# Performance work log

Hardware: AMD Instinct MI355X
Metric: run time of the kernel (lower is better)

## Reference

```python
import jax, jax.numpy as jnp
import numpy as np


def setup_inputs() -> dict:
    key = jax.random.key(0)
    k1, k2, k3, k4 = jax.random.split(key, 4)
    B, T, F, U = 64, 1024, 256, 512
    x = jax.random.normal(k1, (B, T, F), dtype=jnp.float32)
    # small init scale keeps the linear-activation cell state numerically tame
    kernel = jax.random.normal(k2, (F, 4 * U), dtype=jnp.float32) * 0.05
    recurrent_kernel = jax.random.normal(k3, (U, 4 * U), dtype=jnp.float32) * 0.05
    bias = jax.random.normal(k4, (4 * U,), dtype=jnp.float32) * 0.05
    return {"x": x, "kernel": kernel, "recurrent_kernel": recurrent_kernel, "bias": bias}


def reference(x, kernel, recurrent_kernel, bias):
    # Keras LSTM with activation=None (linear candidate / linear output),
    # recurrent_activation=sigmoid, gate order [i, f, c, o]; then external tanh.
    B, T, F = x.shape
    U = recurrent_kernel.shape[0]
    # precompute input projections for all timesteps: [T, B, 4U]
    xz = jnp.einsum('btf,fg->tbg', x, kernel) + bias

    def step(carry, xz_t):
        h, c = carry
        z = xz_t + h @ recurrent_kernel  # [B, 4U]
        i, f, g, o = jnp.split(z, 4, axis=-1)
        i = jax.nn.sigmoid(i)
        f = jax.nn.sigmoid(f)
        o = jax.nn.sigmoid(o)
        c = f * c + i * g          # candidate activation is linear (None)
        h = o * c                  # output activation is linear (None)
        return (h, c), h

    h0 = jnp.zeros((B, U), dtype=x.dtype)
    c0 = jnp.zeros((B, U), dtype=x.dtype)
    (_, _), hs = jax.lax.scan(step, (h0, c0), xz)  # hs: [T, B, U]
    seq = jnp.swapaxes(hs, 0, 1)  # [B, T, U] (return_sequences=True)
    return jnp.tanh(seq)          # external activation applied post-hoc
```

## Files before the change

### kernel.cpp

```cpp
#include <hip/hip_runtime.h>
#include <stdint.h>


#define Tt   1024
#define Uu   512
#define G4U  2048
#define NWG  256
#define NTHR 128
#define TAGSTRIDE 16

#define WF_ELEMS (2 * 24 * 64 * 8)
#define WF_BYTES (WF_ELEMS * 2)
#define ZB_PLANE (16 * 17)
#define SMEM_BYTES (WF_BYTES + 4 * ZB_PLANE * 4)

typedef short  bf16x8 __attribute__((ext_vector_type(8)));
typedef float  f32x4  __attribute__((ext_vector_type(4)));
typedef int    int4v  __attribute__((ext_vector_type(4)));
typedef unsigned int u32;

__device__ __forceinline__ unsigned short f2bf(float f) {
  u32 u = __builtin_bit_cast(u32, f);
  u += 0x7fffu + ((u >> 16) & 1u);
  return (unsigned short)(u >> 16);
}

__device__ __forceinline__ int4v load16_ag(const unsigned short* p) {
  int4v r;
  asm volatile("global_load_dwordx4 %0, %1, off sc1"
               : "=v"(r) : "v"(p) : "memory");
  return r;
}
__device__ __forceinline__ void store2_ag(unsigned short* p, unsigned short v) {
  asm volatile("global_store_short %0, %1, off sc1"
               :: "v"(p), "v"((u32)v) : "memory");
}
__device__ __forceinline__ void store4_ag(u32* p, u32 v) {
  asm volatile("global_store_dword %0, %1, off sc1"
               :: "v"(p), "v"(v) : "memory");
}
__device__ __forceinline__ u32 load_tag_wait(const u32* p) {
  u32 r;
  asm volatile("global_load_dword %0, %1, off sc1\n\ts_waitcnt vmcnt(0)"
               : "=v"(r) : "v"(p) : "memory");
  return r;
}

__device__ __forceinline__ float sigf(float z) {
  return __builtin_amdgcn_rcpf(1.f + __expf(-z));
}
__device__ __forceinline__ float tanh_fast(float v) {
  const float e = __expf(-2.f * fabsf(v));
  const float r = (1.f - e) * __builtin_amdgcn_rcpf(1.f + e);
  return copysignf(r, v);
}

extern "C" __global__ void __launch_bounds__(NTHR, 1)
lstm_persistent(const float* __restrict__ x,
                const float* __restrict__ Wk,
                const float* __restrict__ Rk,
                const float* __restrict__ bias,
                float* __restrict__ out,
                unsigned short* __restrict__ hbuf,
                u32* __restrict__ tags)
{
  extern __shared__ char smem[];
  unsigned short* wf   = (unsigned short*)smem;
  float*          zbuf = (float*)(smem + WF_BYTES);

  const int bid = blockIdx.x;
  const int tid = threadIdx.x;
  const int w   = tid >> 6;
  const int l   = tid & 63;
  const int g   = bid & 3;
  const int m   = bid >> 2;

  for (int i = tid; i < WF_ELEMS; i += NTHR) {
    const int j    = i & 7;
    const int lane = (i >> 3) & 63;
    const int kt   = (i >> 9) % 24;
    const int nt   = (i >> 9) / 24;
    const int k    = kt * 32 + ((lane >> 4) << 3) + j;
    const int n    = nt * 16 + (lane & 15);
    const int zc   = (n >> 3) * Uu + m * 8 + (n & 7);
    const float v  = (k < 256) ? Wk[(size_t)k * G4U + zc]
                               : Rk[(size_t)(k - 256) * G4U + zc];
    wf[i] = f2bf(v);
  }
  __syncthreads();

  bf16x8 wfx[4][2];
  #pragma unroll
  for (int q = 0; q < 4; ++q)
    #pragma unroll
    for (int nt = 0; nt < 2; ++nt)
      wfx[q][nt] = *(const bf16x8*)(wf + (((nt * 24) + (2 * q + w)) * 64 + l) * 8);

  const int row_c = tid >> 3;
  const int uu    = tid & 7;
  const int b_out = g * 16 + row_c;
  const int u_out = m * 8 + uu;
  float breg[4];
  #pragma unroll
  for (int gg = 0; gg < 4; ++gg) breg[gg] = bias[gg * Uu + u_out];
  float creg = 0.f;

  const int b_ld = g * 16 + (l & 15);
  const int kq   = (l >> 4) * 8;
  const u32* tagp = tags + ((size_t)g * 64 + l) * TAGSTRIDE;

  for (int t = 0; t < Tt; ++t) {
    u32 tv = (u32)t;
    if (w == 0)
      asm volatile("global_load_dword %0, %1, off sc1"
                   : "=v"(tv) : "v"(tagp) : "memory");

    f32x4 aX0 = {0.f, 0.f, 0.f, 0.f};
    f32x4 aX1 = {0.f, 0.f, 0.f, 0.f};
    const float* xp = x + ((size_t)b_ld * Tt + t) * 256 + kq;
    #pragma unroll
    for (int q = 0; q < 4; ++q) {
      const int kt = 2 * q + w;
      const float4 v0 = *(const float4*)(xp + kt * 32);
      const float4 v1 = *(const float4*)(xp + kt * 32 + 4);
      int r0, r1, r2, r3;
      asm("v_cvt_pk_bf16_f32 %0, %1, %2" : "=v"(r0) : "v"(v0.x), "v"(v0.y));
      asm("v_cvt_pk_bf16_f32 %0, %1, %2" : "=v"(r1) : "v"(v0.z), "v"(v0.w));
      asm("v_cvt_pk_bf16_f32 %0, %1, %2" : "=v"(r2) : "v"(v1.x), "v"(v1.y));
      asm("v_cvt_pk_bf16_f32 %0, %1, %2" : "=v"(r3) : "v"(v1.z), "v"(v1.w));
      const int4v ai = {r0, r1, r2, r3};
      const bf16x8 a = __builtin_bit_cast(bf16x8, ai);
      aX0 = __builtin_amdgcn_mfma_f32_16x16x32_bf16(a, wfx[q][0], aX0, 0, 0, 0);
      aX1 = __builtin_amdgcn_mfma_f32_16x16x32_bf16(a, wfx[q][1], aX1, 0, 0, 0);
    }

    asm volatile("s_waitcnt vmcnt(0)" ::: "memory");
    __builtin_amdgcn_sched_barrier(0);
    if (w == 0) {
      while (!__all(tv >= (u32)t)) {
        __builtin_amdgcn_s_sleep(1);
        tv = load_tag_wait(tagp);
        __builtin_amdgcn_sched_barrier(0);
      }
    }
    __builtin_amdgcn_s_barrier();
    __builtin_amdgcn_sched_barrier(0);

    const unsigned short* hrow =
        hbuf + ((size_t)(t & 1) * 64 + b_ld) * Uu + kq;
    int4v hf[8];
    #pragma unroll
    for (int q = 0; q < 8; ++q)
      hf[q] = load16_ag(hrow + (2 * q + w) * 32);
    asm volatile("s_waitcnt vmcnt(0)" ::: "memory");
    __builtin_amdgcn_sched_barrier(0);

    f32x4 aH0 = {0.f, 0.f, 0.f, 0.f};
    f32x4 aH1 = {0.f, 0.f, 0.f, 0.f};
    #pragma unroll
    for (int q = 0; q < 8; ++q) {
      const int kt = 8 + 2 * q + w;
      const bf16x8 a = __builtin_bit_cast(bf16x8, hf[q]);
      const bf16x8 b0 = *(const bf16x8*)(wf + ((0 * 24 + kt) * 64 + l) * 8);
      const bf16x8 b1 = *(const bf16x8*)(wf + ((1 * 24 + kt) * 64 + l) * 8);
      aH0 = __builtin_amdgcn_mfma_f32_16x16x32_bf16(a, b0, aH0, 0, 0, 0);
      aH1 = __builtin_amdgcn_mfma_f32_16x16x32_bf16(a, b1, aH1, 0, 0, 0);
    }

    const f32x4 z0 = aX0 + aH0;
    const f32x4 z1 = aX1 + aH1;

    __syncthreads();
    {
      float* zb = zbuf + ((w * 2 + 0) * 16 + (l >> 4) * 4) * 17 + (l & 15);
      #pragma unroll
      for (int r = 0; r < 4; ++r) {
        zb[r * 17]           = z0[r];
        zb[r * 17 + 16 * 17] = z1[r];
      }
    }
    __syncthreads();

    float z[4];
    #pragma unroll
    for (int gg = 0; gg < 4; ++gg) {
      const int n  = gg * 8 + uu;
      const int nt = n >> 4, nc = n & 15;
      z[gg] = zbuf[((0 + nt) * 16 + row_c) * 17 + nc]
            + zbuf[((2 + nt) * 16 + row_c) * 17 + nc]
            + breg[gg];
    }
    const float ig = sigf(z[0]);
    const float fg = sigf(z[1]);
    const float og = sigf(z[3]);
    const float cc = fg * creg + ig * z[2];
    creg = cc;
    const float hh = og * cc;

    store2_ag(hbuf + ((size_t)((t + 1) & 1) * 64 + b_out) * Uu + u_out,
              f2bf(hh));
    asm volatile("s_waitcnt vmcnt(0)" ::: "memory");
    __builtin_amdgcn_sched_barrier(0);
    __builtin_amdgcn_s_barrier();
    if (tid == 0)
      store4_ag(tags + ((size_t)g * 64 + m) * TAGSTRIDE, (u32)(t + 1));

    __builtin_nontemporal_store(tanh_fast(hh),
                                &out[((size_t)b_out * Tt + t) * Uu + u_out]);
  }
}

extern "C" void kernel_launch(void* const* d_in, const int* in_sizes, int n_in,
                              void* d_out, int out_size, void* d_ws, size_t ws_size,
                              hipStream_t stream) {
  const float* x    = (const float*)d_in[0];
  const float* Wk   = (const float*)d_in[1];
  const float* Rk   = (const float*)d_in[2];
  const float* bias = (const float*)d_in[3];
  float* out = (float*)d_out;
  unsigned short* hbuf = (unsigned short*)d_ws;
  u32* tags = (u32*)((char*)d_ws + (size_t)2 * 64 * Uu * sizeof(unsigned short));

  hipMemsetAsync(d_ws, 0,
                 (size_t)2 * 64 * Uu * sizeof(unsigned short)
                   + (size_t)4 * 64 * TAGSTRIDE * sizeof(u32),
                 stream);

  (void)hipFuncSetAttribute((const void*)lstm_persistent,
                            hipFuncAttributeMaxDynamicSharedMemorySize,
                            SMEM_BYTES);

  hipLaunchKernelGGL(lstm_persistent, dim3(NWG), dim3(NTHR), SMEM_BYTES, stream,
                     x, Wk, Rk, bias, out, hbuf, tags);
}
```

Baseline: 3.271 ms.

## Prefetch next-step x and tag loads, double-buffer z scratch to drop a barrier

Software-pipelines the persistent LSTM loop. The next timestep's x tile is loaded during the h-load and MFMA phase, and the tag poll for the next step is issued right after the tag store. This keeps global latency off the critical recurrent path. The z LDS scratch is double-buffered by step parity, so the leading __syncthreads is removed. The changes rely on hand-placed vmcnt counts and add register pressure for the prefetched x data, so a miscounted wait could read stale data.

```diff
diff --git a/kernel.cpp b/kernel.cpp
--- a/kernel.cpp
+++ b/kernel.cpp
@@ -12,7 +12,8 @@
 #define WF_ELEMS (2 * 24 * 64 * 8)
 #define WF_BYTES (WF_ELEMS * 2)
 #define ZB_PLANE (16 * 17)
-#define SMEM_BYTES (WF_BYTES + 4 * ZB_PLANE * 4)
+#define ZB_HALF  (4 * ZB_PLANE)
+#define SMEM_BYTES (WF_BYTES + 2 * ZB_HALF * 4)
 
 typedef short  bf16x8 __attribute__((ext_vector_type(8)));
 typedef float  f32x4  __attribute__((ext_vector_type(4)));
@@ -25,12 +26,18 @@
   return (unsigned short)(u >> 16);
 }
 
-__device__ __forceinline__ int4v load16_ag(const unsigned short* p) {
+__device__ __forceinline__ int4v ld16_ag(const unsigned short* p) {
   int4v r;
   asm volatile("global_load_dwordx4 %0, %1, off sc1"
                : "=v"(r) : "v"(p) : "memory");
   return r;
 }
+__device__ __forceinline__ int4v ld16_nc(const float* p) {
+  int4v r;
+  asm volatile("global_load_dwordx4 %0, %1, off"
+               : "=v"(r) : "v"(p) : "memory");
+  return r;
+}
 __device__ __forceinline__ void store2_ag(unsigned short* p, unsigned short v) {
   asm volatile("global_store_short %0, %1, off sc1"
                :: "v"(p), "v"((u32)v) : "memory");
@@ -38,12 +45,6 @@
 __device__ __forceinline__ void store4_ag(u32* p, u32 v) {
   asm volatile("global_store_dword %0, %1, off sc1"
                :: "v"(p), "v"(v) : "memory");
-}
-__device__ __forceinline__ u32 load_tag_wait(const u32* p) {
-  u32 r;
-  asm volatile("global_load_dword %0, %1, off sc1\n\ts_waitcnt vmcnt(0)"
-               : "=v"(r) : "v"(p) : "memory");
-  return r;
 }
 
 __device__ __forceinline__ float sigf(float z) {
@@ -109,37 +110,48 @@
   const int kq   = (l >> 4) * 8;
   const u32* tagp = tags + ((size_t)g * 64 + l) * TAGSTRIDE;
 
+  int4v xv[4][2];
+  {
+    const float* xp0 = x + ((size_t)b_ld * Tt + 0) * 256 + kq;
+    #pragma unroll
+    for (int q = 0; q < 4; ++q) {
+      const int kt = 2 * q + w;
+      xv[q][0] = ld16_nc(xp0 + kt * 32);
+      xv[q][1] = ld16_nc(xp0 + kt * 32 + 4);
+    }
+  }
+  u32 tv = 0;
+  if (w == 0)
+    asm volatile("global_load_dword %0, %1, off sc1"
+                 : "=v"(tv) : "v"(tagp) : "memory");
+  asm volatile("s_waitcnt vmcnt(0)" ::: "memory");
+  __builtin_amdgcn_sched_barrier(0);
+
   for (int t = 0; t < Tt; ++t) {
-    u32 tv = (u32)t;
-    if (w == 0)
-      asm volatile("global_load_dword %0, %1, off sc1"
-                   : "=v"(tv) : "v"(tagp) : "memory");
-
     f32x4 aX0 = {0.f, 0.f, 0.f, 0.f};
     f32x4 aX1 = {0.f, 0.f, 0.f, 0.f};
-    const float* xp = x + ((size_t)b_ld * Tt + t) * 256 + kq;
     #pragma unroll
     for (int q = 0; q < 4; ++q) {
-      const int kt = 2 * q + w;
-      const float4 v0 = *(const float4*)(xp + kt * 32);
-      const float4 v1 = *(const float4*)(xp + kt * 32 + 4);
+      const f32x4 v0 = __builtin_bit_cast(f32x4, xv[q][0]);
+      const f32x4 v1 = __builtin_bit_cast(f32x4, xv[q][1]);
       int r0, r1, r2, r3;
-      asm("v_cvt_pk_bf16_f32 %0, %1, %2" : "=v"(r0) : "v"(v0.x), "v"(v0.y));
-      asm("v_cvt_pk_bf16_f32 %0, %1, %2" : "=v"(r1) : "v"(v0.z), "v"(v0.w));
-      asm("v_cvt_pk_bf16_f32 %0, %1, %2" : "=v"(r2) : "v"(v1.x), "v"(v1.y));
-      asm("v_cvt_pk_bf16_f32 %0, %1, %2" : "=v"(r3) : "v"(v1.z), "v"(v1.w));
+      asm("v_cvt_pk_bf16_f32 %0, %1, %2" : "=v"(r0) : "v"(v0[0]), "v"(v0[1]));
+      asm("v_cvt_pk_bf16_f32 %0, %1, %2" : "=v"(r1) : "v"(v0[2]), "v"(v0[3]));
+      asm("v_cvt_pk_bf16_f32 %0, %1, %2" : "=v"(r2) : "v"(v1[0]), "v"(v1[1]));
+      asm("v_cvt_pk_bf16_f32 %0, %1, %2" : "=v"(r3) : "v"(v1[2]), "v"(v1[3]));
       const int4v ai = {r0, r1, r2, r3};
       const bf16x8 a = __builtin_bit_cast(bf16x8, ai);
       aX0 = __builtin_amdgcn_mfma_f32_16x16x32_bf16(a, wfx[q][0], aX0, 0, 0, 0);
       aX1 = __builtin_amdgcn_mfma_f32_16x16x32_bf16(a, wfx[q][1], aX1, 0, 0, 0);
     }
 
-    asm volatile("s_waitcnt vmcnt(0)" ::: "memory");
-    __builtin_amdgcn_sched_barrier(0);
     if (w == 0) {
+      asm volatile("s_waitcnt vmcnt(1)" ::: "memory");
+      __builtin_amdgcn_sched_barrier(0);
       while (!__all(tv >= (u32)t)) {
         __builtin_amdgcn_s_sleep(1);
-        tv = load_tag_wait(tagp);
+        asm volatile("global_load_dword %0, %1, off sc1\n\ts_waitcnt vmcnt(0)"
+                     : "=v"(tv) : "v"(tagp) : "memory");
         __builtin_amdgcn_sched_barrier(0);
       }
     }
@@ -151,14 +163,24 @@
     int4v hf[8];
     #pragma unroll
     for (int q = 0; q < 8; ++q)
-      hf[q] = load16_ag(hrow + (2 * q + w) * 32);
-    asm volatile("s_waitcnt vmcnt(0)" ::: "memory");
-    __builtin_amdgcn_sched_barrier(0);
+      hf[q] = ld16_ag(hrow + (2 * q + w) * 32);
+    {
+      const int tn = (t + 1 < Tt) ? t + 1 : t;
+      const float* xpn = x + ((size_t)b_ld * Tt + tn) * 256 + kq;
+      #pragma unroll
+      for (int q = 0; q < 4; ++q) {
+        const int kt = 2 * q + w;
+        xv[q][0] = ld16_nc(xpn + kt * 32);
+        xv[q][1] = ld16_nc(xpn + kt * 32 + 4);
+      }
+    }
 
     f32x4 aH0 = {0.f, 0.f, 0.f, 0.f};
     f32x4 aH1 = {0.f, 0.f, 0.f, 0.f};
-    #pragma unroll
-    for (int q = 0; q < 8; ++q) {
+    asm volatile("s_waitcnt vmcnt(12)" ::: "memory");
+    __builtin_amdgcn_sched_barrier(0);
+    #pragma unroll
+    for (int q = 0; q < 4; ++q) {
       const int kt = 8 + 2 * q + w;
       const bf16x8 a = __builtin_bit_cast(bf16x8, hf[q]);
       const bf16x8 b0 = *(const bf16x8*)(wf + ((0 * 24 + kt) * 64 + l) * 8);
@@ -166,17 +188,28 @@
       aH0 = __builtin_amdgcn_mfma_f32_16x16x32_bf16(a, b0, aH0, 0, 0, 0);
       aH1 = __builtin_amdgcn_mfma_f32_16x16x32_bf16(a, b1, aH1, 0, 0, 0);
     }
+    asm volatile("s_waitcnt vmcnt(8)" ::: "memory");
+    __builtin_amdgcn_sched_barrier(0);
+    #pragma unroll
+    for (int q = 4; q < 8; ++q) {
+      const int kt = 8 + 2 * q + w;
+      const bf16x8 a = __builtin_bit_cast(bf16x8, hf[q]);
+      const bf16x8 b0 = *(const bf16x8*)(wf + ((0 * 24 + kt) * 64 + l) * 8);
+      const bf16x8 b1 = *(const bf16x8*)(wf + ((1 * 24 + kt) * 64 + l) * 8);
+      aH0 = __builtin_amdgcn_mfma_f32_16x16x32_bf16(a, b0, aH0, 0, 0, 0);
+      aH1 = __builtin_amdgcn_mfma_f32_16x16x32_bf16(a, b1, aH1, 0, 0, 0);
+    }
 
     const f32x4 z0 = aX0 + aH0;
     const f32x4 z1 = aX1 + aH1;
 
-    __syncthreads();
+    float* zb = zbuf + (t & 1) * ZB_HALF;
     {
-      float* zb = zbuf + ((w * 2 + 0) * 16 + (l >> 4) * 4) * 17 + (l & 15);
+      float* zw = zb + ((w * 2 + 0) * 16 + (l >> 4) * 4) * 17 + (l & 15);
       #pragma unroll
       for (int r = 0; r < 4; ++r) {
-        zb[r * 17]           = z0[r];
-        zb[r * 17 + 16 * 17] = z1[r];
+        zw[r * 17]           = z0[r];
+        zw[r * 17 + 16 * 17] = z1[r];
       }
     }
     __syncthreads();
@@ -186,8 +219,8 @@
     for (int gg = 0; gg < 4; ++gg) {
       const int n  = gg * 8 + uu;
       const int nt = n >> 4, nc = n & 15;
-      z[gg] = zbuf[((0 + nt) * 16 + row_c) * 17 + nc]
-            + zbuf[((2 + nt) * 16 + row_c) * 17 + nc]
+      z[gg] = zb[((0 + nt) * 16 + row_c) * 17 + nc]
+            + zb[((2 + nt) * 16 + row_c) * 17 + nc]
             + breg[gg];
     }
     const float ig = sigf(z[0]);
@@ -202,11 +235,18 @@
     asm volatile("s_waitcnt vmcnt(0)" ::: "memory");
     __builtin_amdgcn_sched_barrier(0);
     __builtin_amdgcn_s_barrier();
+    __builtin_amdgcn_sched_barrier(0);
     if (tid == 0)
       store4_ag(tags + ((size_t)g * 64 + m) * TAGSTRIDE, (u32)(t + 1));
-
-    __builtin_nontemporal_store(tanh_fast(hh),
-                                &out[((size_t)b_out * Tt + t) * Uu + u_out]);
+    if (w == 0)
+      asm volatile("global_load_dword %0, %1, off sc1"
+                   : "=v"(tv) : "v"(tagp) : "memory");
+    {
+      const float ov = tanh_fast(hh);
+      float* op = out + ((size_t)b_out * Tt + t) * Uu + u_out;
+      asm volatile("global_store_dword %0, %1, off nt"
+                   :: "v"(op), "v"(ov) : "memory");
+    }
   }
 }
 
@@ -221,10 +261,10 @@
   unsigned short* hbuf = (unsigned short*)d_ws;
   u32* tags = (u32*)((char*)d_ws + (size_t)2 * 64 * Uu * sizeof(unsigned short));
 
-  hipMemsetAsync(d_ws, 0,
-                 (size_t)2 * 64 * Uu * sizeof(unsigned short)
-                   + (size_t)4 * 64 * TAGSTRIDE * sizeof(u32),
-                 stream);
+  (void)hipMemsetAsync(d_ws, 0,
+                       (size_t)2 * 64 * Uu * sizeof(unsigned short)
+                         + (size_t)4 * 64 * TAGSTRIDE * sizeof(u32),
+                       stream);
 
   (void)hipFuncSetAttribute((const void*)lstm_persistent,
                             hipFuncAttributeMaxDynamicSharedMemorySize,
```

New measurement: 2.753 ms, median of 2. -15.8%, faster.
